# Optimization experiments

Hardware: AMD Instinct MI355X
Metric: run time of the kernel (lower is better)

The kernel has to match this reference:

```python
import jax, jax.numpy as jnp
import numpy as np

N_NODES = 20000
E_PER_REL = 100000
IN_DIM = 512
H = 2
C1 = 512  # conv1 out per head -> concat 1024
C2 = 128  # conv2 out per head -> concat 256
NEG_SLOPE = 0.2


def _glorot(key, shape):
    fan_in, fan_out = shape[-1], shape[0]
    lim = jnp.sqrt(6.0 / (fan_in + fan_out))
    return jax.random.uniform(key, shape, jnp.float32, -lim, lim)


def setup_inputs() -> dict:
    key = jax.random.key(0)
    ks = jax.random.split(key, 20)
    inp = {"x": jax.random.normal(ks[0], (N_NODES, IN_DIM), jnp.float32)}
    for i in range(6):
        inp[f"e{i}"] = jax.random.randint(ks[1 + i], (2, E_PER_REL), 0, N_NODES, jnp.int64)
    inp["W1_src"] = _glorot(ks[7], (H * C1, IN_DIM))
    inp["W1_dst"] = _glorot(ks[8], (H * C1, IN_DIM))
    inp["a1_src"] = _glorot(ks[9], (H, C1))
    inp["a1_dst"] = _glorot(ks[10], (H, C1))
    inp["b1"] = jnp.zeros((H * C1,), jnp.float32)
    inp["W2_src"] = _glorot(ks[11], (H * C2, H * C1))
    inp["W2_dst"] = _glorot(ks[12], (H * C2, H * C1))
    inp["a2_src"] = _glorot(ks[13], (H, C2))
    inp["a2_dst"] = _glorot(ks[14], (H, C2))
    inp["b2"] = jnp.zeros((H * C2,), jnp.float32)
    return inp


def gat_conv(x, edge_index, W_src, W_dst, a_src, a_dst, bias, heads, out_ch):
    """PyG GATConv: lin (no bias), per-head additive attention, softmax over dst,
    scatter-sum, concat heads, add bias. add_self_loops=True."""
    N = x.shape[0]
    loops = jnp.arange(N, dtype=edge_index.dtype)
    src = jnp.concatenate([edge_index[0], loops])
    dst = jnp.concatenate([edge_index[1], loops])
    xs = (x @ W_src.T).reshape(N, heads, out_ch)
    xd = (x @ W_dst.T).reshape(N, heads, out_ch)
    al_src = jnp.einsum('nhc,hc->nh', xs, a_src)  # [N,H]
    al_dst = jnp.einsum('nhc,hc->nh', xd, a_dst)
    e = jax.nn.leaky_relu(al_src[src] + al_dst[dst], NEG_SLOPE)  # [E,H]
    # numerically stable segment softmax over incoming edges of each dst node
    m = jax.ops.segment_max(e, dst, num_segments=N)  # self-loops => no empty segments
    p = jnp.exp(e - m[dst])
    s = jax.ops.segment_sum(p, dst, num_segments=N)
    alpha = p / (s[dst] + 1e-16)
    out = jax.ops.segment_sum(xs[src] * alpha[:, :, None], dst, num_segments=N)  # [N,H,C]
    return out.reshape(N, heads * out_ch) + bias


def hetero_layer(x, edges, W_src, W_dst, a_src, a_dst, bias, heads, out_ch):
    # HeteroConv(aggr='sum') with the SAME conv shared across all 6 relations
    out = None
    for e in edges:
        o = gat_conv(x, e, W_src, W_dst, a_src, a_dst, bias, heads, out_ch)
        out = o if out is None else out + o
    return out


def reference(x, e0, e1, e2, e3, e4, e5,
              W1_src, W1_dst, a1_src, a1_dst, b1,
              W2_src, W2_dst, a2_src, a2_dst, b2):
    edges = [e0, e1, e2, e3, e4, e5]
    h = hetero_layer(x, edges, W1_src, W1_dst, a1_src, a1_dst, b1, H, C1)
    h = jax.nn.relu(h)
    out = hetero_layer(h, edges, W2_src, W2_dst, a2_src, a2_dst, b2, H, C2)
    return out  # x_dict['capec'], shape [N, 256]
```

## Files before the change

kernel.cpp:

```cpp
#include <hip/hip_runtime.h>
#include <cstddef>

#define NN 20000
#define EE 100000
#define NR 6
#define HH 2
#define NEG 0.2f
#define NB ((NN + 1023) / 1024)

struct EdgePtrs { const int* e[NR]; };

typedef __attribute__((ext_vector_type(8))) short bf16x8;
typedef __attribute__((ext_vector_type(4))) float f32x4;

__device__ __forceinline__ unsigned short rnebf(float f) {
    unsigned u = __float_as_uint(f);
    return (unsigned short)((u + 0x7fffu + ((u >> 16) & 1u)) >> 16);
}
__device__ __forceinline__ void unpack8(uint4 v, float* f) {
    f[0] = __uint_as_float(v.x << 16); f[1] = __uint_as_float(v.x & 0xffff0000u);
    f[2] = __uint_as_float(v.y << 16); f[3] = __uint_as_float(v.y & 0xffff0000u);
    f[4] = __uint_as_float(v.z << 16); f[5] = __uint_as_float(v.z & 0xffff0000u);
    f[6] = __uint_as_float(v.w << 16); f[7] = __uint_as_float(v.w & 0xffff0000u);
}
__device__ __forceinline__ unsigned pack2(float a, float b) {
    return (unsigned)rnebf(a) | ((unsigned)rnebf(b) << 16);
}
__device__ __forceinline__ float lrelu(float l) { return l > 0.f ? l : NEG * l; }
__device__ __forceinline__ void glld16(unsigned short* lds, const void* g) {
    __builtin_amdgcn_global_load_lds(
        (const __attribute__((address_space(1))) unsigned int*)g,
        (__attribute__((address_space(3))) unsigned int*)lds, 16, 0, 0);
}

__global__ void f2b_all(const float* __restrict__ x, unsigned short* __restrict__ xb, int nx,
                        const float* __restrict__ w1, unsigned short* __restrict__ wb1, int nw1,
                        const float* __restrict__ w2, unsigned short* __restrict__ wb2, int nw2) {
    int i = (blockIdx.x * 256 + threadIdx.x) * 4;
    const float* in; unsigned short* out; int k;
    if (i < nx) { in = x; out = xb; k = i; }
    else if (i < nx + nw1) { in = w1; out = wb1; k = i - nx; }
    else if (i < nx + nw1 + nw2) { in = w2; out = wb2; k = i - nx - nw1; }
    else return;
    float4 v = *(const float4*)&in[k];
    unsigned short o[4] = {rnebf(v.x), rnebf(v.y), rnebf(v.z), rnebf(v.w)};
    *(uint2*)&out[k] = *(uint2*)o;
}

__global__ void fold_a2_kernel(const float* __restrict__ Wa, const float* __restrict__ aa,
                               float* __restrict__ wta,
                               const float* __restrict__ Wb, const float* __restrict__ ab,
                               float* __restrict__ wtb, int C, int K) {
    __shared__ float red[256];
    const float* W = blockIdx.z ? Wb : Wa;
    const float* a = blockIdx.z ? ab : aa;
    float* wt      = blockIdx.z ? wtb : wta;
    int h = blockIdx.y;
    int k = blockIdx.x * 64 + (threadIdx.x & 63);
    int cp = threadIdx.x >> 6;
    float acc = 0.f;
    for (int c = cp; c < C; c += 4)
        acc = fmaf(a[h * C + c], W[(size_t)(h * C + c) * K + k], acc);
    red[threadIdx.x] = acc;
    __syncthreads();
    if (cp == 0) {
        acc = red[threadIdx.x] + red[threadIdx.x + 64] +
              red[threadIdx.x + 128] + red[threadIdx.x + 192];
        wt[h * K + k] = acc;
    }
}

template <int BN, bool FUSEAL>
__global__ __launch_bounds__(256) void gemm_nt_mfma(
    const unsigned short* __restrict__ A, const unsigned short* __restrict__ B,
    unsigned short* __restrict__ C, int M, int Nn, int K,
    const float* __restrict__ a1s, float* __restrict__ as1) {
    constexpr int NF = BN / 32;
    __shared__ unsigned short As[128 * 32];
    __shared__ unsigned short Bs[BN * 32];
    const int tid = threadIdx.x;
    const int lane = tid & 63;
    const int wave = tid >> 6;
    const int wr = wave >> 1, wc = wave & 1;
    const int row0 = blockIdx.y * 128, col0 = blockIdx.x * BN;

    f32x4 acc[4][NF];
#pragma unroll
    for (int i = 0; i < 4; ++i)
#pragma unroll
        for (int j = 0; j < NF; ++j) acc[i][j] = (f32x4){0.f, 0.f, 0.f, 0.f};

    const int srow = tid >> 2;
    const int slot = tid & 3;
    const int sw = ((slot ^ (srow & 3)) << 4);
    int ar0 = row0 + srow;        if (ar0 >= M) ar0 = M - 1;
    int ar1 = row0 + srow + 64;   if (ar1 >= M) ar1 = M - 1;
    const int br0 = col0 + srow;
    const int br1 = col0 + srow + 64;

    const int q = lane >> 4;
    for (int k0 = 0; k0 < K; k0 += 32) {
        glld16(As + tid * 8,        (const char*)A + ((size_t)ar0 * K + k0) * 2 + sw);
        glld16(As + tid * 8 + 2048, (const char*)A + ((size_t)ar1 * K + k0) * 2 + sw);
        glld16(Bs + tid * 8,        (const char*)B + ((size_t)br0 * K + k0) * 2 + sw);
        if (BN == 128)
            glld16(Bs + tid * 8 + 2048, (const char*)B + ((size_t)br1 * K + k0) * 2 + sw);
        __syncthreads();
        bf16x8 af[4], bfr[NF];
#pragma unroll
        for (int m = 0; m < 4; ++m) {
            int r = wr * 64 + m * 16 + (lane & 15);
            af[m] = *(const bf16x8*)&As[r * 32 + ((q ^ (r & 3)) << 3)];
        }
#pragma unroll
        for (int nI = 0; nI < NF; ++nI) {
            int c = wc * (BN / 2) + nI * 16 + (lane & 15);
            bfr[nI] = *(const bf16x8*)&Bs[c * 32 + ((q ^ (c & 3)) << 3)];
        }
#pragma unroll
        for (int m = 0; m < 4; ++m)
#pragma unroll
            for (int nI = 0; nI < NF; ++nI)
                acc[m][nI] = __builtin_amdgcn_mfma_f32_16x16x32_bf16(af[m], bfr[nI], acc[m][nI], 0, 0, 0);
        __syncthreads();
    }
    const int crow = (lane >> 4) * 4;
    const int ccol = lane & 15;
#pragma unroll
    for (int m = 0; m < 4; ++m)
#pragma unroll
        for (int nI = 0; nI < NF; ++nI)
#pragma unroll
            for (int j = 0; j < 4; ++j) {
                int r = row0 + wr * 64 + m * 16 + crow + j;
                int c = col0 + wc * (BN / 2) + nI * 16 + ccol;
                if (r < M) C[(size_t)r * Nn + c] = rnebf(acc[m][nI][j]);
            }
    if constexpr (FUSEAL) {
        const int hb = col0 >> 9;
        float aS[NF];
#pragma unroll
        for (int nI = 0; nI < NF; ++nI) {
            int gc = col0 + wc * (BN / 2) + nI * 16 + ccol;
            aS[nI] = a1s[hb * 512 + (gc & 511)];
        }
#pragma unroll
        for (int m = 0; m < 4; ++m)
#pragma unroll
            for (int j = 0; j < 4; ++j) {
                float ps = 0.f;
#pragma unroll
                for (int nI = 0; nI < NF; ++nI)
                    ps = fmaf(acc[m][nI][j], aS[nI], ps);
                for (int o = 1; o < 16; o <<= 1)
                    ps += __shfl_xor(ps, o);
                if ((lane & 15) == 0) {
                    int r = row0 + wr * 64 + m * 16 + crow + j;
                    if (r < M) atomicAdd(&as1[r * 2 + hb], ps);
                }
            }
    }
}

__global__ void al_dst_w(const unsigned short* __restrict__ x, const float* __restrict__ wtd,
                         int K, float* __restrict__ ad) {
    int lane = threadIdx.x & 63;
    int n = blockIdx.x * 4 + (threadIdx.x >> 6);
    if (n >= NN) return;
    float d0 = 0.f, d1 = 0.f;
    for (int k0 = 0; k0 < K; k0 += 512) {
        int k = k0 + lane * 8;
        uint4 xv = *(const uint4*)&x[(size_t)n * K + k];
        float xf[8];
        unpack8(xv, xf);
        float4 wda = *(const float4*)&wtd[k],     wdb = *(const float4*)&wtd[k + 4];
        float4 wdc = *(const float4*)&wtd[K + k], wdd = *(const float4*)&wtd[K + k + 4];
        d0 = fmaf(xf[0], wda.x, d0); d0 = fmaf(xf[1], wda.y, d0);
        d0 = fmaf(xf[2], wda.z, d0); d0 = fmaf(xf[3], wda.w, d0);
        d0 = fmaf(xf[4], wdb.x, d0); d0 = fmaf(xf[5], wdb.y, d0);
        d0 = fmaf(xf[6], wdb.z, d0); d0 = fmaf(xf[7], wdb.w, d0);
        d1 = fmaf(xf[0], wdc.x, d1); d1 = fmaf(xf[1], wdc.y, d1);
        d1 = fmaf(xf[2], wdc.z, d1); d1 = fmaf(xf[3], wdc.w, d1);
        d1 = fmaf(xf[4], wdd.x, d1); d1 = fmaf(xf[5], wdd.y, d1);
        d1 = fmaf(xf[6], wdd.z, d1); d1 = fmaf(xf[7], wdd.w, d1);
    }
    for (int o = 32; o > 0; o >>= 1) {
        d0 += __shfl_down(d0, o); d1 += __shfl_down(d1, o);
    }
    if (lane == 0) {
        ad[n * 2 + 0] = d0;
        ad[n * 2 + 1] = d1;
    }
}

__global__ void count_kernel(EdgePtrs ep, int* __restrict__ count) {
    int i = blockIdx.x * 256 + threadIdx.x;
    if (i >= NR * EE) return;
    int r = i / EE, ei = i - r * EE;
    atomicAdd(&count[ep.e[r][EE + ei]], 1);
}

__global__ void scatter_static(EdgePtrs ep, int* __restrict__ cursor, int2* __restrict__ recs) {
    int i = blockIdx.x * 256 + threadIdx.x;
    if (i >= NR * EE) return;
    int r = i / EE, ei = i - r * EE;
    int sN = ep.e[r][ei];
    int d = ep.e[r][EE + ei];
    int slot = atomicAdd(&cursor[d], 1);
    recs[slot] = make_int2(sN, r);
}

__global__ void block_sum(const int* __restrict__ count, int* __restrict__ bsum) {
    int base = blockIdx.x * 1024;
    int tid = threadIdx.x;
    int s = 0;
    for (int i = tid; i < 1024; i += 256) {
        int idx = base + i;
        s += (idx < NN) ? count[idx] : 0;
    }
    for (int o = 32; o > 0; o >>= 1) s += __shfl_down(s, o);
    __shared__ int ws[4];
    if ((tid & 63) == 0) ws[tid >> 6] = s;
    __syncthreads();
    if (tid == 0) bsum[blockIdx.x] = ws[0] + ws[1] + ws[2] + ws[3];
}

__global__ void scan_small(const int* __restrict__ bsum, int* __restrict__ bbase,
                           int* __restrict__ offs) {
    if (threadIdx.x == 0) {
        int run = 0;
        for (int i = 0; i < NB; ++i) { bbase[i] = run; run += bsum[i]; }
        offs[NN] = run;
    }
}

__global__ void scan_blocks(const int* __restrict__ count, const int* __restrict__ bbase,
                            int* __restrict__ offs, int* __restrict__ cursor) {
    __shared__ int wsum[16];
    __shared__ int wbase[16];
    int tid = threadIdx.x;
    int lane = tid & 63;
    int wid = tid >> 6;
    int idx = blockIdx.x * 1024 + tid;
    int v = (idx < NN) ? count[idx] : 0;
    int xv = v;
    for (int d = 1; d < 64; d <<= 1) {
        int t = __shfl_up(xv, d);
        if (lane >= d) xv += t;
    }
    if (lane == 63) wsum[wid] = xv;
    __syncthreads();
    if (wid == 0 && lane < 16) {
        int wv = wsum[lane];
        int wx = wv;
        for (int d = 1; d < 16; d <<= 1) {
            int t = __shfl_up(wx, d);
            if (lane >= d) wx += t;
        }
        wbase[lane] = wx - wv;
    }
    __syncthreads();
    int excl = xv - v + wbase[wid] + bbase[blockIdx.x];
    if (idx < NN) { offs[idx] = excl; cursor[idx] = excl; }
}

__global__ __launch_bounds__(64) void aggregate_l1f(
    const unsigned short* __restrict__ xs, const int2* __restrict__ recs,
    const int* __restrict__ offs,
    const float* __restrict__ als, const float* __restrict__ ald,
    const float* __restrict__ bias,
    const float* __restrict__ wts2, const float* __restrict__ wtd2,
    float* __restrict__ as2, float* __restrict__ ad2,
    unsigned short* __restrict__ out) {
    __shared__ float s_loc[NR];
    int bid = blockIdx.x;
    int n = bid >> 1;
    int half = bid & 1;
    int t = threadIdx.x;
    int c0 = half * 512 + t * 8;
    float ad_n = ald[n * 2 + half];
    float els = expf(lrelu(als[n * 2 + half] + ad_n));
    if (t < NR) s_loc[t] = els;
    __syncthreads();
    int beg = offs[n], end = offs[n + 1];
    for (int j = beg + t; j < end; j += 64) {
        int2 rc = recs[j];
        atomicAdd(&s_loc[rc.y], expf(lrelu(als[rc.x * 2 + half] + ad_n)));
    }
    __syncthreads();
    if (t < NR) s_loc[t] = 1.f / (s_loc[t] + 1e-16f);
    __syncthreads();
    float rsum = s_loc[0] + s_loc[1] + s_loc[2] + s_loc[3] + s_loc[4] + s_loc[5];
    float coef = els * rsum;
    float a0[8], a1[8], f[8];
    uint4 sv = *(const uint4*)&xs[(size_t)n * 1024 + c0];
    unpack8(sv, f);
#pragma unroll
    for (int j = 0; j < 8; ++j) {
        a0[j] = coef * f[j] + 6.f * bias[c0 + j];
        a1[j] = 0.f;
    }
    int j = beg;
    for (; j + 1 < end; j += 2) {
        int2 r0 = recs[j], r1 = recs[j + 1];
        uint4 v0 = *(const uint4*)&xs[(size_t)r0.x * 1024 + c0];
        uint4 v1 = *(const uint4*)&xs[(size_t)r1.x * 1024 + c0];
        float l0 = lrelu(als[r0.x * 2 + half] + ad_n);
        float l1 = lrelu(als[r1.x * 2 + half] + ad_n);
        float al0 = expf(l0) * s_loc[r0.y];
        float al1 = expf(l1) * s_loc[r1.y];
        unpack8(v0, f);
#pragma unroll
        for (int q = 0; q < 8; ++q) a0[q] = fmaf(al0, f[q], a0[q]);
        unpack8(v1, f);
#pragma unroll
        for (int q = 0; q < 8; ++q) a1[q] = fmaf(al1, f[q], a1[q]);
    }
    if (j < end) {
        int2 r0 = recs[j];
        uint4 v0 = *(const uint4*)&xs[(size_t)r0.x * 1024 + c0];
        float l0 = lrelu(als[r0.x * 2 + half] + ad_n);
        float al0 = expf(l0) * s_loc[r0.y];
        unpack8(v0, f);
#pragma unroll
        for (int q = 0; q < 8; ++q) a0[q] = fmaf(al0, f[q], a0[q]);
    }
    float rr[8];
#pragma unroll
    for (int q = 0; q < 8; ++q) rr[q] = fmaxf(a0[q] + a1[q], 0.f);
    uint4 o;
    o.x = pack2(rr[0], rr[1]); o.y = pack2(rr[2], rr[3]);
    o.z = pack2(rr[4], rr[5]); o.w = pack2(rr[6], rr[7]);
    *(uint4*)&out[(size_t)n * 1024 + c0] = o;
    float ps0, ps1, pd0, pd1;
    float4 wsa = *(const float4*)&wts2[c0],        wsb = *(const float4*)&wts2[c0 + 4];
    float4 wsc = *(const float4*)&wts2[1024 + c0], wsd = *(const float4*)&wts2[1024 + c0 + 4];
    float4 wda = *(const float4*)&wtd2[c0],        wdb = *(const float4*)&wtd2[c0 + 4];
    float4 wdc = *(const float4*)&wtd2[1024 + c0], wdd = *(const float4*)&wtd2[1024 + c0 + 4];
    ps0 = rr[0]*wsa.x + rr[1]*wsa.y + rr[2]*wsa.z + rr[3]*wsa.w
        + rr[4]*wsb.x + rr[5]*wsb.y + rr[6]*wsb.z + rr[7]*wsb.w;
    ps1 = rr[0]*wsc.x + rr[1]*wsc.y + rr[2]*wsc.z + rr[3]*wsc.w
        + rr[4]*wsd.x + rr[5]*wsd.y + rr[6]*wsd.z + rr[7]*wsd.w;
    pd0 = rr[0]*wda.x + rr[1]*wda.y + rr[2]*wda.z + rr[3]*wda.w
        + rr[4]*wdb.x + rr[5]*wdb.y + rr[6]*wdb.z + rr[7]*wdb.w;
    pd1 = rr[0]*wdc.x + rr[1]*wdc.y + rr[2]*wdc.z + rr[3]*wdc.w
        + rr[4]*wdd.x + rr[5]*wdd.y + rr[6]*wdd.z + rr[7]*wdd.w;
    for (int o2 = 32; o2 > 0; o2 >>= 1) {
        ps0 += __shfl_down(ps0, o2); ps1 += __shfl_down(ps1, o2);
        pd0 += __shfl_down(pd0, o2); pd1 += __shfl_down(pd1, o2);
    }
    if (t == 0) {
        atomicAdd(&as2[n * 2 + 0], ps0);
        atomicAdd(&as2[n * 2 + 1], ps1);
        atomicAdd(&ad2[n * 2 + 0], pd0);
        atomicAdd(&ad2[n * 2 + 1], pd1);
    }
}

__global__ __launch_bounds__(64) void aggregate_l2(
    const unsigned short* __restrict__ xs, const int2* __restrict__ recs,
    const int* __restrict__ offs,
    const float* __restrict__ als, const float* __restrict__ ald,
    const float* __restrict__ bias, float* __restrict__ out) {
    __shared__ float s_loc[NR * HH];
    int n = blockIdx.x;
    int t = threadIdx.x;
    int h = t >> 5;
    float ad_n = ald[n * 2 + h];
    float els = expf(lrelu(als[n * 2 + h] + ad_n));
    if (t < NR * HH) s_loc[t] = expf(lrelu(als[n * 2 + (t & 1)] + ald[n * 2 + (t & 1)]));
    __syncthreads();
    int beg = offs[n], end = offs[n + 1];
    for (int j = beg + (t & 31); j < end; j += 32) {
        int2 rc = recs[j];
        atomicAdd(&s_loc[rc.y * 2 + h], expf(lrelu(als[rc.x * 2 + h] + ad_n)));
    }
    __syncthreads();
    if (t < NR * HH) s_loc[t] = 1.f / (s_loc[t] + 1e-16f);
    __syncthreads();
    float rsum = s_loc[0 + h] + s_loc[2 + h] + s_loc[4 + h] +
                 s_loc[6 + h] + s_loc[8 + h] + s_loc[10 + h];
    float coef = els * rsum;
    float a0[4], a1[4];
    uint2 sv = *(const uint2*)&xs[(size_t)n * 256 + t * 4];
    a0[0] = coef * __uint_as_float(sv.x << 16)          + 6.f * bias[t * 4 + 0];
    a0[1] = coef * __uint_as_float(sv.x & 0xffff0000u)  + 6.f * bias[t * 4 + 1];
    a0[2] = coef * __uint_as_float(sv.y << 16)          + 6.f * bias[t * 4 + 2];
    a0[3] = coef * __uint_as_float(sv.y & 0xffff0000u)  + 6.f * bias[t * 4 + 3];
#pragma unroll
    for (int q = 0; q < 4; ++q) a1[q] = 0.f;
    int j = beg;
    for (; j + 1 < end; j += 2) {
        int2 r0 = recs[j], r1 = recs[j + 1];
        uint2 v0 = *(const uint2*)&xs[(size_t)r0.x * 256 + t * 4];
        uint2 v1 = *(const uint2*)&xs[(size_t)r1.x * 256 + t * 4];
        float l0 = lrelu(als[r0.x * 2 + h] + ad_n);
        float l1 = lrelu(als[r1.x * 2 + h] + ad_n);
        float al0 = expf(l0) * s_loc[r0.y * 2 + h];
        float al1 = expf(l1) * s_loc[r1.y * 2 + h];
        a0[0] = fmaf(al0, __uint_as_float(v0.x << 16), a0[0]);
        a0[1] = fmaf(al0, __uint_as_float(v0.x & 0xffff0000u), a0[1]);
        a0[2] = fmaf(al0, __uint_as_float(v0.y << 16), a0[2]);
        a0[3] = fmaf(al0, __uint_as_float(v0.y & 0xffff0000u), a0[3]);
        a1[0] = fmaf(al1, __uint_as_float(v1.x << 16), a1[0]);
        a1[1] = fmaf(al1, __uint_as_float(v1.x & 0xffff0000u), a1[1]);
        a1[2] = fmaf(al1, __uint_as_float(v1.y << 16), a1[2]);
        a1[3] = fmaf(al1, __uint_as_float(v1.y & 0xffff0000u), a1[3]);
    }
    if (j < end) {
        int2 r0 = recs[j];
        uint2 v0 = *(const uint2*)&xs[(size_t)r0.x * 256 + t * 4];
        float l0 = lrelu(als[r0.x * 2 + h] + ad_n);
        float al0 = expf(l0) * s_loc[r0.y * 2 + h];
        a0[0] = fmaf(al0, __uint_as_float(v0.x << 16), a0[0]);
        a0[1] = fmaf(al0, __uint_as_float(v0.x & 0xffff0000u), a0[1]);
        a0[2] = fmaf(al0, __uint_as_float(v0.y << 16), a0[2]);
        a0[3] = fmaf(al0, __uint_as_float(v0.y & 0xffff0000u), a0[3]);
    }
    float4 o = make_float4(a0[0] + a1[0], a0[1] + a1[1], a0[2] + a1[2], a0[3] + a1[3]);
    *(float4*)&out[(size_t)n * 256 + t * 4] = o;
}

extern "C" void kernel_launch(void* const* d_in, const int* in_sizes, int n_in,
                              void* d_out, int out_size, void* d_ws, size_t ws_size,
                              hipStream_t stream) {
    const float* x = (const float*)d_in[0];
    EdgePtrs ep;
    for (int r = 0; r < NR; ++r) ep.e[r] = (const int*)d_in[1 + r];
    const float* W1s = (const float*)d_in[7];
    const float* W1d = (const float*)d_in[8];
    const float* a1s = (const float*)d_in[9];
    const float* a1d = (const float*)d_in[10];
    const float* b1  = (const float*)d_in[11];
    const float* W2s = (const float*)d_in[12];
    const float* W2d = (const float*)d_in[13];
    const float* a2s = (const float*)d_in[14];
    const float* a2d = (const float*)d_in[15];
    const float* b2  = (const float*)d_in[16];
    float* out = (float*)d_out;

    char* base = (char*)d_ws;
    size_t off = 0;
    auto take = [&](size_t nbytes) -> void* {
        void* p = base + off;
        off = (off + nbytes + 255) & ~(size_t)255;
        return p;
    };
    unsigned short* xb   = (unsigned short*)take((size_t)NN * 512 * 2);
    unsigned short* xs1b = (unsigned short*)take((size_t)NN * 1024 * 2);
    unsigned short* h1b  = (unsigned short*)take((size_t)NN * 1024 * 2);
    unsigned short* xs2b = xs1b;
    unsigned short* Wb1  = (unsigned short*)take((size_t)1024 * 512 * 2);
    unsigned short* Wb2  = (unsigned short*)take((size_t)256 * 1024 * 2);
    float* as1   = (float*)take((size_t)NN * HH * 4);
    float* ad1   = (float*)take((size_t)NN * HH * 4);
    float* as2   = (float*)take((size_t)NN * HH * 4);
    float* ad2   = (float*)take((size_t)NN * HH * 4);
    int* count   = (int*)take((size_t)NN * 4);
    int* offs    = (int*)take((size_t)(NN + 1) * 4);
    int* cursor  = (int*)take((size_t)NN * 4);
    int2* recs   = (int2*)take((size_t)NR * EE * 8);
    float* wts   = (float*)take((size_t)HH * 1024 * 4);
    float* wtd   = (float*)take((size_t)HH * 1024 * 4);
    int* bsum    = (int*)take((size_t)NB * 4);
    int* bbase   = (int*)take((size_t)NB * 4);

    const int EB = (NR * EE + 255) / 256;
    const int NX = NN * 512, NW1 = 1024 * 512, NW2 = 256 * 1024;

    hipMemsetAsync(as1, 0, (size_t)4 * NN * HH * 4 + (size_t)NN * 4, stream);

    {
        const int K = 512, Nout = 1024;
        f2b_all<<<((NX + NW1 + NW2) / 4 + 255) / 256, 256, 0, stream>>>(
            x, xb, NX, W1s, Wb1, NW1, W2s, Wb2, NW2);
        gemm_nt_mfma<128, true><<<dim3(Nout / 128, (NN + 127) / 128), 256, 0, stream>>>(
            xb, Wb1, xs1b, NN, Nout, K, a1s, as1);
        fold_a2_kernel<<<dim3(K / 64, HH, 1), 256, 0, stream>>>(W1d, a1d, wtd,
                                                                nullptr, nullptr, nullptr, 512, K);
        al_dst_w<<<(NN + 3) / 4, 256, 0, stream>>>(xb, wtd, K, ad1);
        count_kernel<<<EB, 256, 0, stream>>>(ep, count);
        block_sum<<<NB, 256, 0, stream>>>(count, bsum);
        scan_small<<<1, 64, 0, stream>>>(bsum, bbase, offs);
        scan_blocks<<<NB, 1024, 0, stream>>>(count, bbase, offs, cursor);
        scatter_static<<<EB, 256, 0, stream>>>(ep, cursor, recs);
        fold_a2_kernel<<<dim3(1024 / 64, HH, 2), 256, 0, stream>>>(W2s, a2s, wts, W2d, a2d, wtd, 128, 1024);
        aggregate_l1f<<<NN * 2, 64, 0, stream>>>(xs1b, recs, offs, as1, ad1,
                                                 b1, wts, wtd, as2, ad2, h1b);
    }
    {
        const int K = 1024, Nout = 256;
        gemm_nt_mfma<64, false><<<dim3(Nout / 64, (NN + 127) / 128), 256, 0, stream>>>(
            h1b, Wb2, xs2b, NN, Nout, K, nullptr, nullptr);
        aggregate_l2<<<NN, 64, 0, stream>>>(xs2b, recs, offs, as2, ad2, b2, out);
    }
}
```

Baseline: 426.8 us.

## Merge small setup kernels to cut launch count

Folds the edge-count pass into the bf16 conversion kernel, merges the two weight-fold launches into one grid, and replaces the three-kernel prefix scan with one extra block appended to the dst-attention kernel. The goal is to drop several tiny launches and their serialization gaps. The single-block scan is serial per thread over 79 entries and may sit on the critical path as a straggler block.

```diff
diff --git a/kernel.cpp b/kernel.cpp
--- a/kernel.cpp
+++ b/kernel.cpp
@@ -6,7 +6,6 @@
 #define NR 6
 #define HH 2
 #define NEG 0.2f
-#define NB ((NN + 1023) / 1024)
 
 struct EdgePtrs { const int* e[NR]; };
 
@@ -33,10 +32,20 @@
         (__attribute__((address_space(3))) unsigned int*)lds, 16, 0, 0);
 }
 
-__global__ void f2b_all(const float* __restrict__ x, unsigned short* __restrict__ xb, int nx,
-                        const float* __restrict__ w1, unsigned short* __restrict__ wb1, int nw1,
-                        const float* __restrict__ w2, unsigned short* __restrict__ wb2, int nw2) {
-    int i = (blockIdx.x * 256 + threadIdx.x) * 4;
+__global__ void f2b_count(const float* __restrict__ x, unsigned short* __restrict__ xb, int nx,
+                          const float* __restrict__ w1, unsigned short* __restrict__ wb1, int nw1,
+                          const float* __restrict__ w2, unsigned short* __restrict__ wb2, int nw2,
+                          int fb, EdgePtrs ep, int* __restrict__ count) {
+    int b = blockIdx.x;
+    if (b >= fb) {
+        int i = (b - fb) * 256 + threadIdx.x;
+        if (i < NR * EE) {
+            int r = i / EE, ei = i - r * EE;
+            atomicAdd(&count[ep.e[r][EE + ei]], 1);
+        }
+        return;
+    }
+    int i = (b * 256 + threadIdx.x) * 4;
     const float* in; unsigned short* out; int k;
     if (i < nx) { in = x; out = xb; k = i; }
     else if (i < nx + nw1) { in = w1; out = wb1; k = i - nx; }
@@ -47,16 +56,20 @@
     *(uint2*)&out[k] = *(uint2*)o;
 }
 
-__global__ void fold_a2_kernel(const float* __restrict__ Wa, const float* __restrict__ aa,
-                               float* __restrict__ wta,
-                               const float* __restrict__ Wb, const float* __restrict__ ab,
-                               float* __restrict__ wtb, int C, int K) {
+__global__ void fold_all(const float* __restrict__ W1d, const float* __restrict__ a1d,
+                         float* __restrict__ wtd1,
+                         const float* __restrict__ W2s, const float* __restrict__ a2s,
+                         float* __restrict__ wts2,
+                         const float* __restrict__ W2d, const float* __restrict__ a2d,
+                         float* __restrict__ wtd2) {
     __shared__ float red[256];
-    const float* W = blockIdx.z ? Wb : Wa;
-    const float* a = blockIdx.z ? ab : aa;
-    float* wt      = blockIdx.z ? wtb : wta;
+    const float *W, *a; float* wt; int C, K;
+    if (blockIdx.z == 0)      { W = W1d; a = a1d; wt = wtd1; C = 512; K = 512; }
+    else if (blockIdx.z == 1) { W = W2s; a = a2s; wt = wts2; C = 128; K = 1024; }
+    else                      { W = W2d; a = a2d; wt = wtd2; C = 128; K = 1024; }
     int h = blockIdx.y;
     int k = blockIdx.x * 64 + (threadIdx.x & 63);
+    if (k >= K) return;
     int cp = threadIdx.x >> 6;
     float acc = 0.f;
     for (int c = cp; c < C; c += 4)
@@ -64,9 +77,8 @@
     red[threadIdx.x] = acc;
     __syncthreads();
     if (cp == 0) {
-        acc = red[threadIdx.x] + red[threadIdx.x + 64] +
-              red[threadIdx.x + 128] + red[threadIdx.x + 192];
-        wt[h * K + k] = acc;
+        wt[h * K + k] = red[threadIdx.x] + red[threadIdx.x + 64] +
+                        red[threadIdx.x + 128] + red[threadIdx.x + 192];
     }
 }
 
@@ -162,8 +174,48 @@
     }
 }
 
-__global__ void al_dst_w(const unsigned short* __restrict__ x, const float* __restrict__ wtd,
-                         int K, float* __restrict__ ad) {
+__global__ void al_dst_scan(const unsigned short* __restrict__ x, const float* __restrict__ wtd,
+                            int K, float* __restrict__ ad,
+                            const int* __restrict__ count, int* __restrict__ offs,
+                            int* __restrict__ cursor) {
+    if (blockIdx.x == gridDim.x - 1) {
+        __shared__ int wsum[4], wbase[4];
+        int tid = threadIdx.x;
+        const int C = 79;
+        int base = tid * C;
+        int sum = 0;
+        for (int i = 0; i < C; ++i) {
+            int idx = base + i;
+            if (idx < NN) sum += count[idx];
+        }
+        int lane = tid & 63, wid = tid >> 6;
+        int xv = sum;
+        for (int d = 1; d < 64; d <<= 1) {
+            int t2 = __shfl_up(xv, d);
+            if (lane >= d) xv += t2;
+        }
+        if (lane == 63) wsum[wid] = xv;
+        __syncthreads();
+        if (tid == 0) {
+            wbase[0] = 0;
+            wbase[1] = wsum[0];
+            wbase[2] = wsum[0] + wsum[1];
+            wbase[3] = wsum[0] + wsum[1] + wsum[2];
+        }
+        __syncthreads();
+        int excl = (xv - sum) + wbase[wid];
+        for (int i = 0; i < C; ++i) {
+            int idx = base + i;
+            if (idx < NN) {
+                int v = count[idx];
+                offs[idx] = excl;
+                cursor[idx] = excl;
+                excl += v;
+            }
+        }
+        if (tid == 255) offs[NN] = excl;
+        return;
+    }
     int lane = threadIdx.x & 63;
     int n = blockIdx.x * 4 + (threadIdx.x >> 6);
     if (n >= NN) return;
@@ -193,13 +245,6 @@
     }
 }
 
-__global__ void count_kernel(EdgePtrs ep, int* __restrict__ count) {
-    int i = blockIdx.x * 256 + threadIdx.x;
-    if (i >= NR * EE) return;
-    int r = i / EE, ei = i - r * EE;
-    atomicAdd(&count[ep.e[r][EE + ei]], 1);
-}
-
 __global__ void scatter_static(EdgePtrs ep, int* __restrict__ cursor, int2* __restrict__ recs) {
     int i = blockIdx.x * 256 + threadIdx.x;
     if (i >= NR * EE) return;
@@ -208,60 +253,6 @@
     int d = ep.e[r][EE + ei];
     int slot = atomicAdd(&cursor[d], 1);
     recs[slot] = make_int2(sN, r);
-}
-
-__global__ void block_sum(const int* __restrict__ count, int* __restrict__ bsum) {
-    int base = blockIdx.x * 1024;
-    int tid = threadIdx.x;
-    int s = 0;
-    for (int i = tid; i < 1024; i += 256) {
-        int idx = base + i;
-        s += (idx < NN) ? count[idx] : 0;
-    }
-    for (int o = 32; o > 0; o >>= 1) s += __shfl_down(s, o);
-    __shared__ int ws[4];
-    if ((tid & 63) == 0) ws[tid >> 6] = s;
-    __syncthreads();
-    if (tid == 0) bsum[blockIdx.x] = ws[0] + ws[1] + ws[2] + ws[3];
-}
-
-__global__ void scan_small(const int* __restrict__ bsum, int* __restrict__ bbase,
-                           int* __restrict__ offs) {
-    if (threadIdx.x == 0) {
-        int run = 0;
-        for (int i = 0; i < NB; ++i) { bbase[i] = run; run += bsum[i]; }
-        offs[NN] = run;
-    }
-}
-
-__global__ void scan_blocks(const int* __restrict__ count, const int* __restrict__ bbase,
-                            int* __restrict__ offs, int* __restrict__ cursor) {
-    __shared__ int wsum[16];
-    __shared__ int wbase[16];
-    int tid = threadIdx.x;
-    int lane = tid & 63;
-    int wid = tid >> 6;
-    int idx = blockIdx.x * 1024 + tid;
-    int v = (idx < NN) ? count[idx] : 0;
-    int xv = v;
-    for (int d = 1; d < 64; d <<= 1) {
-        int t = __shfl_up(xv, d);
-        if (lane >= d) xv += t;
-    }
-    if (lane == 63) wsum[wid] = xv;
-    __syncthreads();
-    if (wid == 0 && lane < 16) {
-        int wv = wsum[lane];
-        int wx = wv;
-        for (int d = 1; d < 16; d <<= 1) {
-            int t = __shfl_up(wx, d);
-            if (lane >= d) wx += t;
-        }
-        wbase[lane] = wx - wv;
-    }
-    __syncthreads();
-    int excl = xv - v + wbase[wid] + bbase[blockIdx.x];
-    if (idx < NN) { offs[idx] = excl; cursor[idx] = excl; }
 }
 
 __global__ __launch_bounds__(64) void aggregate_l1f(
@@ -460,33 +451,29 @@
     int* offs    = (int*)take((size_t)(NN + 1) * 4);
     int* cursor  = (int*)take((size_t)NN * 4);
     int2* recs   = (int2*)take((size_t)NR * EE * 8);
-    float* wts   = (float*)take((size_t)HH * 1024 * 4);
-    float* wtd   = (float*)take((size_t)HH * 1024 * 4);
-    int* bsum    = (int*)take((size_t)NB * 4);
-    int* bbase   = (int*)take((size_t)NB * 4);
+    float* wtd1  = (float*)take((size_t)HH * 512 * 4);
+    float* wts2  = (float*)take((size_t)HH * 1024 * 4);
+    float* wtd2  = (float*)take((size_t)HH * 1024 * 4);
 
     const int EB = (NR * EE + 255) / 256;
     const int NX = NN * 512, NW1 = 1024 * 512, NW2 = 256 * 1024;
+    const int FB = ((NX + NW1 + NW2) / 4 + 255) / 256;
 
     hipMemsetAsync(as1, 0, (size_t)4 * NN * HH * 4 + (size_t)NN * 4, stream);
 
     {
         const int K = 512, Nout = 1024;
-        f2b_all<<<((NX + NW1 + NW2) / 4 + 255) / 256, 256, 0, stream>>>(
-            x, xb, NX, W1s, Wb1, NW1, W2s, Wb2, NW2);
+        f2b_count<<<FB + EB, 256, 0, stream>>>(x, xb, NX, W1s, Wb1, NW1, W2s, Wb2, NW2,
+                                               FB, ep, count);
         gemm_nt_mfma<128, true><<<dim3(Nout / 128, (NN + 127) / 128), 256, 0, stream>>>(
             xb, Wb1, xs1b, NN, Nout, K, a1s, as1);
-        fold_a2_kernel<<<dim3(K / 64, HH, 1), 256, 0, stream>>>(W1d, a1d, wtd,
-                                                                nullptr, nullptr, nullptr, 512, K);
-        al_dst_w<<<(NN + 3) / 4, 256, 0, stream>>>(xb, wtd, K, ad1);
-        count_kernel<<<EB, 256, 0, stream>>>(ep, count);
-        block_sum<<<NB, 256, 0, stream>>>(count, bsum);
-        scan_small<<<1, 64, 0, stream>>>(bsum, bbase, offs);
-        scan_blocks<<<NB, 1024, 0, stream>>>(count, bbase, offs, cursor);
+        fold_all<<<dim3(16, HH, 3), 256, 0, stream>>>(W1d, a1d, wtd1,
+                                                      W2s, a2s, wts2, W2d, a2d, wtd2);
+        al_dst_scan<<<(NN + 3) / 4 + 1, 256, 0, stream>>>(xb, wtd1, K, ad1,
+                                                          count, offs, cursor);
         scatter_static<<<EB, 256, 0, stream>>>(ep, cursor, recs);
-        fold_a2_kernel<<<dim3(1024 / 64, HH, 2), 256, 0, stream>>>(W2s, a2s, wts, W2d, a2d, wtd, 128, 1024);
         aggregate_l1f<<<NN * 2, 64, 0, stream>>>(xs1b, recs, offs, as1, ad1,
-                                                 b1, wts, wtd, as2, ad2, h1b);
+                                                 b1, wts2, wtd2, as2, ad2, h1b);
     }
     {
         const int K = 1024, Nout = 256;
```

Result: slower. 454.5 us (+6.5%).
